# Kernel tuning notes

Measured on AMD Instinct MI355X. Metric: run time of the kernel, lower is better.

Reference implementation:

```python
import jax, jax.numpy as jnp
import numpy as np

IN_FEATURES = 4096
OUT_FEATURES = 11008


def setup_inputs() -> dict:
    key = jax.random.key(0)
    kx, kw, ks, kb = jax.random.split(key, 4)
    x = jax.random.normal(kx, (64, IN_FEATURES), dtype=jnp.float32)
    # int8 quantized weight, stored as int32 for portability (values in [-128, 127])
    weight_quantized = jax.random.randint(kw, (OUT_FEATURES, IN_FEATURES), -128, 128, dtype=jnp.int32)
    # per-tensor scale, as produced by quantize_weights_int8: |w|.max()/127
    weight_scale = jnp.asarray(0.01, dtype=jnp.float32)
    bias = jax.random.normal(kb, (OUT_FEATURES,), dtype=jnp.float32) * 0.02
    return {"x": x, "weight_quantized": weight_quantized, "weight_scale": weight_scale, "bias": bias}


def reference(x, weight_quantized, weight_scale, bias):
    # dequantize_weights_int8: q.float() * scale, then F.linear(x, W, b) = x @ W.T + b
    weight = weight_quantized.astype(jnp.float32) * weight_scale  # [out, in]
    return jnp.einsum('mi,oi->mo', x, weight) + bias
```

## Files before the change

kernel.cpp:

```cpp
#include <hip/hip_runtime.h>


#define M_DIM 64
#define N_DIM 11008
#define K_DIM 4096
#define KSPLIT 8
#define KC (K_DIM / KSPLIT)
#define BK 128
#define BLOCK_N 64

typedef __attribute__((ext_vector_type(8))) short bf16x8;
typedef __attribute__((ext_vector_type(8))) short s16x8;
typedef __attribute__((ext_vector_type(4))) float f32x4;
typedef __attribute__((ext_vector_type(4))) int i32x4;
typedef __attribute__((ext_vector_type(4))) short s16x4;

__device__ __forceinline__ short i2bf(int q) {
    float f = (float)q;
    return (short)(__builtin_bit_cast(unsigned int, f) >> 16);
}

__device__ __forceinline__ short f2bf(float f) {
    unsigned int u = __builtin_bit_cast(unsigned int, f);
    u = u + 0x7FFFu + ((u >> 16) & 1u);
    return (short)(u >> 16);
}

__device__ __forceinline__ void load_lds_16B(const void* g, void* l) {
    __builtin_amdgcn_global_load_lds(
        (const __attribute__((address_space(1))) unsigned int*)g,
        (__attribute__((address_space(3))) unsigned int*)l,
        16, 0, 0);
}

__global__ __launch_bounds__(256) void xcvt_kernel(const float* __restrict__ x,
                                                   short* __restrict__ xbf) {
    int idx = (blockIdx.x * 256 + threadIdx.x) * 8;
    f32x4 a = *(const f32x4*)(x + idx);
    f32x4 b = *(const f32x4*)(x + idx + 4);
    s16x8 h;
    h[0] = f2bf(a.x); h[1] = f2bf(a.y); h[2] = f2bf(a.z); h[3] = f2bf(a.w);
    h[4] = f2bf(b.x); h[5] = f2bf(b.y); h[6] = f2bf(b.z); h[7] = f2bf(b.w);
    *(s16x8*)(xbf + idx) = h;
}

__global__ __launch_bounds__(256) void init_bias_kernel(const float* __restrict__ bias,
                                                        float* __restrict__ out) {
    int idx = blockIdx.x * 256 + threadIdx.x;
    int col4 = idx % 2752;
    f32x4 b = *(const f32x4*)(bias + col4 * 4);
    *(f32x4*)(out + (size_t)idx * 4) = b;
}

__global__ __launch_bounds__(256) void qlinear_v4_kernel(const short* __restrict__ xbf,
                                                         const int* __restrict__ wq,
                                                         const float* __restrict__ scale_p,
                                                         float* __restrict__ out) {
    __shared__ char smem[49152];
    char* wlds = smem;
    char* xlds = smem + 32768;

    const int tid  = threadIdx.x;
    const int wave = tid >> 6;
    const int lane = tid & 63;
    const int quad = lane >> 4;
    const int l16  = lane & 15;

    const int n0  = blockIdx.x * BLOCK_N;
    const int kc0 = blockIdx.y * KC;
    const float scale = *scale_p;

    f32x4 acc[4] = {f32x4{0,0,0,0}, f32x4{0,0,0,0}, f32x4{0,0,0,0}, f32x4{0,0,0,0}};

    for (int kb = 0; kb < KC; kb += BK) {
        #pragma unroll
        for (int j = 0; j < 8; ++j) {
            int row  = wave * 16 + j * 2 + (lane >> 5);
            int colb = ((lane & 31) * 16) ^ ((row & 7) << 4);
            const char* g = (const char*)(wq + (size_t)(n0 + row) * K_DIM + kc0 + kb) + colb;
            load_lds_16B(g, wlds + (wave * 16 + j * 2) * 512);
        }
        #pragma unroll
        for (int j = 0; j < 4; ++j) {
            int row  = wave * 16 + j * 4 + (lane >> 4);
            int colb = ((lane & 15) * 16) ^ ((row & 7) << 4);
            const char* g = (const char*)(xbf + (size_t)row * K_DIM + kc0 + kb) + colb;
            load_lds_16B(g, xlds + (wave * 16 + j * 4) * 256);
        }
        __syncthreads();

        #pragma unroll
        for (int kk = 0; kk < BK; kk += 32) {
            const int wrow = wave * 16 + l16;
            const int wsw  = (wrow & 7) << 4;
            const int L0   = (kk + quad * 8) * 4;
            i32x4 b0 = *(const i32x4*)(wlds + wrow * 512 + ((L0)      ^ wsw));
            i32x4 b1 = *(const i32x4*)(wlds + wrow * 512 + ((L0 + 16) ^ wsw));
            bf16x8 bfrag;
            bfrag[0] = i2bf(b0.x); bfrag[1] = i2bf(b0.y);
            bfrag[2] = i2bf(b0.z); bfrag[3] = i2bf(b0.w);
            bfrag[4] = i2bf(b1.x); bfrag[5] = i2bf(b1.y);
            bfrag[6] = i2bf(b1.z); bfrag[7] = i2bf(b1.w);

            #pragma unroll
            for (int mi = 0; mi < 4; ++mi) {
                const int arow = mi * 16 + l16;
                const int La   = (kk + quad * 8) * 2;
                bf16x8 afrag = *(const bf16x8*)(xlds + arow * 256 + (La ^ ((arow & 7) << 4)));
                acc[mi] = __builtin_amdgcn_mfma_f32_16x16x32_bf16(afrag, bfrag, acc[mi], 0, 0, 0);
            }
        }
        __syncthreads();
    }

    const int nout = n0 + wave * 16 + l16;
    #pragma unroll
    for (int mi = 0; mi < 4; ++mi) {
        #pragma unroll
        for (int r = 0; r < 4; ++r) {
            int m = mi * 16 + quad * 4 + r;
            atomicAdd(&out[(size_t)m * N_DIM + nout], acc[mi][r] * scale);
        }
    }
}

#define LDS_STRIDE 136

__global__ __launch_bounds__(256) void qlinear_atomic_kernel(const float* __restrict__ x,
                                                             const int* __restrict__ wq,
                                                             const float* __restrict__ scale_p,
                                                             float* __restrict__ out) {
    __shared__ short lds[M_DIM * LDS_STRIDE];

    const int tid  = threadIdx.x;
    const int wave = tid >> 6;
    const int lane = tid & 63;
    const int quad = lane >> 4;
    const int l16  = lane & 15;

    const int n0  = blockIdx.x * BLOCK_N;
    const int kc0 = blockIdx.y * KC;
    const float scale = *scale_p;

    const int nw = n0 + wave * 16 + l16;
    const int* wptr = wq + (size_t)nw * K_DIM + kc0 + quad * 8;

    f32x4 acc[4] = {f32x4{0,0,0,0}, f32x4{0,0,0,0}, f32x4{0,0,0,0}, f32x4{0,0,0,0}};

    for (int kb = 0; kb < KC; kb += BK) {
        {
            const float* xbase = x + kc0 + kb;
            #pragma unroll
            for (int j = 0; j < 8; ++j) {
                int f  = tid + j * 256;
                int row = f >> 5;
                int c4  = f & 31;
                f32x4 v = *(const f32x4*)(xbase + (size_t)row * K_DIM + c4 * 4);
                s16x4 h;
                h.x = f2bf(v.x); h.y = f2bf(v.y); h.z = f2bf(v.z); h.w = f2bf(v.w);
                *(s16x4*)&lds[row * LDS_STRIDE + c4 * 4] = h;
            }
        }
        __syncthreads();

        #pragma unroll
        for (int kk = 0; kk < BK; kk += 32) {
            i32x4 b0 = *(const i32x4*)(wptr + kb + kk);
            i32x4 b1 = *(const i32x4*)(wptr + kb + kk + 4);
            bf16x8 bfrag;
            bfrag[0] = i2bf(b0.x); bfrag[1] = i2bf(b0.y);
            bfrag[2] = i2bf(b0.z); bfrag[3] = i2bf(b0.w);
            bfrag[4] = i2bf(b1.x); bfrag[5] = i2bf(b1.y);
            bfrag[6] = i2bf(b1.z); bfrag[7] = i2bf(b1.w);

            #pragma unroll
            for (int mi = 0; mi < 4; ++mi) {
                bf16x8 afrag = *(const bf16x8*)&lds[(mi * 16 + l16) * LDS_STRIDE + kk + quad * 8];
                acc[mi] = __builtin_amdgcn_mfma_f32_16x16x32_bf16(afrag, bfrag, acc[mi], 0, 0, 0);
            }
        }
        __syncthreads();
    }

    const int nout = n0 + wave * 16 + l16;
    #pragma unroll
    for (int mi = 0; mi < 4; ++mi) {
        #pragma unroll
        for (int r = 0; r < 4; ++r) {
            int m = mi * 16 + quad * 4 + r;
            atomicAdd(&out[(size_t)m * N_DIM + nout], acc[mi][r] * scale);
        }
    }
}

extern "C" void kernel_launch(void* const* d_in, const int* in_sizes, int n_in,
                              void* d_out, int out_size, void* d_ws, size_t ws_size,
                              hipStream_t stream) {
    const float* x      = (const float*)d_in[0];
    const int*   wq     = (const int*)d_in[1];
    const float* scale  = (const float*)d_in[2];
    const float* bias   = (const float*)d_in[3];
    float* out = (float*)d_out;

    const size_t xbf_bytes = (size_t)M_DIM * K_DIM * sizeof(short);
    dim3 grid(N_DIM / BLOCK_N, KSPLIT);

    if (ws_size >= xbf_bytes && d_ws != nullptr) {
        short* xbf = (short*)d_ws;
        xcvt_kernel<<<(M_DIM * K_DIM) / (256 * 8), 256, 0, stream>>>(x, xbf);
        init_bias_kernel<<<688, 256, 0, stream>>>(bias, out);
        qlinear_v4_kernel<<<grid, 256, 0, stream>>>(xbf, wq, scale, out);
    } else {
        init_bias_kernel<<<688, 256, 0, stream>>>(bias, out);
        qlinear_atomic_kernel<<<grid, 256, 0, stream>>>(x, wq, scale, out);
    }
}
```

Measured before the change: 259.2 us.

## Double-buffer LDS tiles with async loads and fuse prep kernels

Replaces the single-buffered GEMM loop with a two-stage LDS pipeline. The next K tile (now 64 wide) is issued via global_load_lds while the current tile is computed, using explicit vmcnt waits and barriers. It also merges the x-to-bf16 conversion and the bias initialisation into one prep kernel, saving a launch. The risks are a wrong vmcnt count and smaller tiles, which mean more barriers per block.

```diff
diff --git a/kernel.cpp b/kernel.cpp
--- a/kernel.cpp
+++ b/kernel.cpp
@@ -6,8 +6,12 @@
 #define K_DIM 4096
 #define KSPLIT 8
 #define KC (K_DIM / KSPLIT)
-#define BK 128
+#define BK 64
+#define NT (KC / BK)
 #define BLOCK_N 64
+#define WBYTES (64 * 256)
+#define XBYTES (64 * 128)
+#define BUFB (WBYTES + XBYTES)
 
 typedef __attribute__((ext_vector_type(8))) short bf16x8;
 typedef __attribute__((ext_vector_type(8))) short s16x8;
@@ -33,16 +37,124 @@
         16, 0, 0);
 }
 
-__global__ __launch_bounds__(256) void xcvt_kernel(const float* __restrict__ x,
-                                                   short* __restrict__ xbf) {
-    int idx = (blockIdx.x * 256 + threadIdx.x) * 8;
-    f32x4 a = *(const f32x4*)(x + idx);
-    f32x4 b = *(const f32x4*)(x + idx + 4);
-    s16x8 h;
-    h[0] = f2bf(a.x); h[1] = f2bf(a.y); h[2] = f2bf(a.z); h[3] = f2bf(a.w);
-    h[4] = f2bf(b.x); h[5] = f2bf(b.y); h[6] = f2bf(b.z); h[7] = f2bf(b.w);
-    *(s16x8*)(xbf + idx) = h;
-}
+__global__ __launch_bounds__(256) void prep_kernel(const float* __restrict__ x,
+                                                   const float* __restrict__ bias,
+                                                   short* __restrict__ xbf,
+                                                   float* __restrict__ out) {
+    int b = blockIdx.x;
+    if (b < 128) {
+        int idx = (b * 256 + threadIdx.x) * 8;
+        f32x4 a = *(const f32x4*)(x + idx);
+        f32x4 c = *(const f32x4*)(x + idx + 4);
+        s16x8 h;
+        h[0] = f2bf(a.x); h[1] = f2bf(a.y); h[2] = f2bf(a.z); h[3] = f2bf(a.w);
+        h[4] = f2bf(c.x); h[5] = f2bf(c.y); h[6] = f2bf(c.z); h[7] = f2bf(c.w);
+        *(s16x8*)(xbf + idx) = h;
+    } else {
+        int idx = (b - 128) * 256 + threadIdx.x;
+        int col4 = idx % 2752;
+        f32x4 v = *(const f32x4*)(bias + col4 * 4);
+        *(f32x4*)(out + (size_t)idx * 4) = v;
+    }
+}
+
+__device__ __forceinline__ void stage_tile(const int* __restrict__ wq,
+                                           const short* __restrict__ xbf,
+                                           char* buf, int n0, int kA,
+                                           int wave, int lane) {
+    char* wl = buf;
+    char* xl = buf + WBYTES;
+    #pragma unroll
+    for (int j = 0; j < 4; ++j) {
+        int row  = wave * 16 + j * 4 + (lane >> 4);
+        int colb = ((lane & 15) * 16) ^ ((row & 7) << 4);
+        const char* g = (const char*)(wq + (size_t)(n0 + row) * K_DIM + kA) + colb;
+        load_lds_16B(g, wl + (wave * 16 + j * 4) * 256);
+    }
+    #pragma unroll
+    for (int j = 0; j < 2; ++j) {
+        int row  = wave * 16 + j * 8 + (lane >> 3);
+        int colb = ((lane & 7) * 16) ^ ((row & 7) << 4);
+        const char* g = (const char*)(xbf + (size_t)row * K_DIM + kA) + colb;
+        load_lds_16B(g, xl + (wave * 16 + j * 8) * 128);
+    }
+}
+
+__device__ __forceinline__ void compute_tile(const char* buf, f32x4 acc[4],
+                                             int wave, int quad, int l16) {
+    const char* wl = buf;
+    const char* xl = buf + WBYTES;
+    const int wrow = wave * 16 + l16;
+    const int wsw  = (wrow & 7) << 4;
+    #pragma unroll
+    for (int kk = 0; kk < BK; kk += 32) {
+        const int L0 = (kk + quad * 8) * 4;
+        i32x4 b0 = *(const i32x4*)(wl + wrow * 256 + ((L0)      ^ wsw));
+        i32x4 b1 = *(const i32x4*)(wl + wrow * 256 + ((L0 + 16) ^ wsw));
+        bf16x8 bfrag;
+        bfrag[0] = i2bf(b0.x); bfrag[1] = i2bf(b0.y);
+        bfrag[2] = i2bf(b0.z); bfrag[3] = i2bf(b0.w);
+        bfrag[4] = i2bf(b1.x); bfrag[5] = i2bf(b1.y);
+        bfrag[6] = i2bf(b1.z); bfrag[7] = i2bf(b1.w);
+        #pragma unroll
+        for (int mi = 0; mi < 4; ++mi) {
+            const int arow = mi * 16 + l16;
+            const int La   = (kk + quad * 8) * 2;
+            bf16x8 afrag = *(const bf16x8*)(xl + arow * 128 + (La ^ ((arow & 7) << 4)));
+            acc[mi] = __builtin_amdgcn_mfma_f32_16x16x32_bf16(afrag, bfrag, acc[mi], 0, 0, 0);
+        }
+    }
+}
+
+__global__ __launch_bounds__(256) void qlinear_v5_kernel(const short* __restrict__ xbf,
+                                                         const int* __restrict__ wq,
+                                                         const float* __restrict__ scale_p,
+                                                         float* __restrict__ out) {
+    __shared__ char smem[2 * BUFB];
+
+    const int tid  = threadIdx.x;
+    const int wave = tid >> 6;
+    const int lane = tid & 63;
+    const int quad = lane >> 4;
+    const int l16  = lane & 15;
+
+    const int n0  = blockIdx.x * BLOCK_N;
+    const int kc0 = blockIdx.y * KC;
+
+    f32x4 acc[4] = {f32x4{0,0,0,0}, f32x4{0,0,0,0}, f32x4{0,0,0,0}, f32x4{0,0,0,0}};
+
+    stage_tile(wq, xbf, smem, n0, kc0, wave, lane);
+
+    for (int t = 0; t < NT - 1; ++t) {
+        char* cur = smem + (t & 1) * BUFB;
+        char* nxt = smem + ((t + 1) & 1) * BUFB;
+        stage_tile(wq, xbf, nxt, n0, kc0 + (t + 1) * BK, wave, lane);
+        asm volatile("s_waitcnt vmcnt(6)" ::: "memory");
+        __builtin_amdgcn_sched_barrier(0);
+        __builtin_amdgcn_s_barrier();
+        compute_tile(cur, acc, wave, quad, l16);
+        __builtin_amdgcn_sched_barrier(0);
+        __builtin_amdgcn_s_barrier();
+    }
+    asm volatile("s_waitcnt vmcnt(0)" ::: "memory");
+    __builtin_amdgcn_sched_barrier(0);
+    __builtin_amdgcn_s_barrier();
+    compute_tile(smem + ((NT - 1) & 1) * BUFB, acc, wave, quad, l16);
+
+    const float scale = *scale_p;
+    const int nout = n0 + wave * 16 + l16;
+    #pragma unroll
+    for (int mi = 0; mi < 4; ++mi) {
+        #pragma unroll
+        for (int r = 0; r < 4; ++r) {
+            int m = mi * 16 + quad * 4 + r;
+            atomicAdd(&out[(size_t)m * N_DIM + nout], acc[mi][r] * scale);
+        }
+    }
+}
+
+#define LDS_STRIDE 136
+#define FB_BK 128
 
 __global__ __launch_bounds__(256) void init_bias_kernel(const float* __restrict__ bias,
                                                         float* __restrict__ out) {
@@ -52,13 +164,11 @@
     *(f32x4*)(out + (size_t)idx * 4) = b;
 }
 
-__global__ __launch_bounds__(256) void qlinear_v4_kernel(const short* __restrict__ xbf,
-                                                         const int* __restrict__ wq,
-                                                         const float* __restrict__ scale_p,
-                                                         float* __restrict__ out) {
-    __shared__ char smem[49152];
-    char* wlds = smem;
-    char* xlds = smem + 32768;
+__global__ __launch_bounds__(256) void qlinear_atomic_kernel(const float* __restrict__ x,
+                                                             const int* __restrict__ wq,
+                                                             const float* __restrict__ scale_p,
+                                                             float* __restrict__ out) {
+    __shared__ short lds[M_DIM * LDS_STRIDE];
 
     const int tid  = threadIdx.x;
     const int wave = tid >> 6;
@@ -70,84 +180,12 @@
     const int kc0 = blockIdx.y * KC;
     const float scale = *scale_p;
 
-    f32x4 acc[4] = {f32x4{0,0,0,0}, f32x4{0,0,0,0}, f32x4{0,0,0,0}, f32x4{0,0,0,0}};
-
-    for (int kb = 0; kb < KC; kb += BK) {
-        #pragma unroll
-        for (int j = 0; j < 8; ++j) {
-            int row  = wave * 16 + j * 2 + (lane >> 5);
-            int colb = ((lane & 31) * 16) ^ ((row & 7) << 4);
-            const char* g = (const char*)(wq + (size_t)(n0 + row) * K_DIM + kc0 + kb) + colb;
-            load_lds_16B(g, wlds + (wave * 16 + j * 2) * 512);
-        }
-        #pragma unroll
-        for (int j = 0; j < 4; ++j) {
-            int row  = wave * 16 + j * 4 + (lane >> 4);
-            int colb = ((lane & 15) * 16) ^ ((row & 7) << 4);
-            const char* g = (const char*)(xbf + (size_t)row * K_DIM + kc0 + kb) + colb;
-            load_lds_16B(g, xlds + (wave * 16 + j * 4) * 256);
-        }
-        __syncthreads();
-
-        #pragma unroll
-        for (int kk = 0; kk < BK; kk += 32) {
-            const int wrow = wave * 16 + l16;
-            const int wsw  = (wrow & 7) << 4;
-            const int L0   = (kk + quad * 8) * 4;
-            i32x4 b0 = *(const i32x4*)(wlds + wrow * 512 + ((L0)      ^ wsw));
-            i32x4 b1 = *(const i32x4*)(wlds + wrow * 512 + ((L0 + 16) ^ wsw));
-            bf16x8 bfrag;
-            bfrag[0] = i2bf(b0.x); bfrag[1] = i2bf(b0.y);
-            bfrag[2] = i2bf(b0.z); bfrag[3] = i2bf(b0.w);
-            bfrag[4] = i2bf(b1.x); bfrag[5] = i2bf(b1.y);
-            bfrag[6] = i2bf(b1.z); bfrag[7] = i2bf(b1.w);
-
-            #pragma unroll
-            for (int mi = 0; mi < 4; ++mi) {
-                const int arow = mi * 16 + l16;
-                const int La   = (kk + quad * 8) * 2;
-                bf16x8 afrag = *(const bf16x8*)(xlds + arow * 256 + (La ^ ((arow & 7) << 4)));
-                acc[mi] = __builtin_amdgcn_mfma_f32_16x16x32_bf16(afrag, bfrag, acc[mi], 0, 0, 0);
-            }
-        }
-        __syncthreads();
-    }
-
-    const int nout = n0 + wave * 16 + l16;
-    #pragma unroll
-    for (int mi = 0; mi < 4; ++mi) {
-        #pragma unroll
-        for (int r = 0; r < 4; ++r) {
-            int m = mi * 16 + quad * 4 + r;
-            atomicAdd(&out[(size_t)m * N_DIM + nout], acc[mi][r] * scale);
-        }
-    }
-}
-
-#define LDS_STRIDE 136
-
-__global__ __launch_bounds__(256) void qlinear_atomic_kernel(const float* __restrict__ x,
-                                                             const int* __restrict__ wq,
-                                                             const float* __restrict__ scale_p,
-                                                             float* __restrict__ out) {
-    __shared__ short lds[M_DIM * LDS_STRIDE];
-
-    const int tid  = threadIdx.x;
-    const int wave = tid >> 6;
-    const int lane = tid & 63;
-    const int quad = lane >> 4;
-    const int l16  = lane & 15;
-
-    const int n0  = blockIdx.x * BLOCK_N;
-    const int kc0 = blockIdx.y * KC;
-    const float scale = *scale_p;
-
     const int nw = n0 + wave * 16 + l16;
     const int* wptr = wq + (size_t)nw * K_DIM + kc0 + quad * 8;
 
     f32x4 acc[4] = {f32x4{0,0,0,0}, f32x4{0,0,0,0}, f32x4{0,0,0,0}, f32x4{0,0,0,0}};
 
-    for (int kb = 0; kb < KC; kb += BK) {
+    for (int kb = 0; kb < KC; kb += FB_BK) {
         {
             const float* xbase = x + kc0 + kb;
             #pragma unroll
@@ -164,7 +202,7 @@
         __syncthreads();
 
         #pragma unroll
-        for (int kk = 0; kk < BK; kk += 32) {
+        for (int kk = 0; kk < FB_BK; kk += 32) {
             i32x4 b0 = *(const i32x4*)(wptr + kb + kk);
             i32x4 b1 = *(const i32x4*)(wptr + kb + kk + 4);
             bf16x8 bfrag;
@@ -207,9 +245,8 @@
 
     if (ws_size >= xbf_bytes && d_ws != nullptr) {
         short* xbf = (short*)d_ws;
-        xcvt_kernel<<<(M_DIM * K_DIM) / (256 * 8), 256, 0, stream>>>(x, xbf);
-        init_bias_kernel<<<688, 256, 0, stream>>>(bias, out);
-        qlinear_v4_kernel<<<grid, 256, 0, stream>>>(xbf, wq, scale, out);
+        prep_kernel<<<816, 256, 0, stream>>>(x, bias, xbf, out);
+        qlinear_v5_kernel<<<grid, 256, 0, stream>>>(xbf, wq, scale, out);
     } else {
         init_bias_kernel<<<688, 256, 0, stream>>>(bias, out);
         qlinear_atomic_kernel<<<grid, 256, 0, stream>>>(x, wq, scale, out);
```

Result: no change. 263.8 us (+1.8%).
